# Kernel optimization log

Measured on AMD Instinct MI355X. Metric: run time of the kernel, lower is better.

The kernel has to match this reference:

```python
import jax, jax.numpy as jnp
import numpy as np

N_NODES = 100000
N_EDGES = 1200000
D_IN = 64
D_HID = 64


def setup_inputs() -> dict:
    key = jax.random.key(0)
    k1, k2, k3, k4, k5 = jax.random.split(key, 5)
    src = jax.random.randint(k1, (N_EDGES,), 0, N_NODES, dtype=jnp.int32)
    dst = jax.random.randint(k2, (N_EDGES,), 0, N_NODES, dtype=jnp.int32)
    w = jax.random.uniform(k3, (N_EDGES,), dtype=jnp.float32)
    data = jax.random.normal(k4, (N_NODES, D_IN), dtype=jnp.float32)
    theta = jax.random.normal(k5, (D_IN, D_HID), dtype=jnp.float32)
    return {"src": src, "dst": dst, "w": w, "data": data, "theta": theta,
            "num_nodes": N_NODES}


def reference(src, dst, w, data, theta, num_nodes):
    # weighted gather of source-node features: [E, D_IN]
    weighted = w[:, None] * data[src]
    # scatter-add into destination nodes: [N, D_IN]
    agg = jax.ops.segment_sum(weighted, dst, num_segments=num_nodes)
    # dense projection: [N, D_HID]
    return jnp.dot(agg, theta)
```

## Files before the change

kernel.cpp:

```cpp
#include <hip/hip_runtime.h>

#define D 64
#define NPB 128
#define NPB_SHIFT 7
#define MAXB 1024
#define SCATTER_T 512
#define CHUNK_MAX 4704
#define SCQ 10
#define CAPB 2560
#define GT 512
#define GQ 5

__device__ inline unsigned f2bf(float f) {
    unsigned u = __float_as_uint(f);
    return (u + 0x7FFFu + ((u >> 16) & 1u)) >> 16;
}

__global__ void zero_i_kernel(int* __restrict__ p, int n) {
    int i = blockIdx.x * blockDim.x + threadIdx.x;
    if (i < n) p[i] = 0;
}
__global__ void zero_f4_kernel(float4* __restrict__ p, int n4) {
    int i = blockIdx.x * blockDim.x + threadIdx.x;
    if (i < n4) p[i] = make_float4(0.f, 0.f, 0.f, 0.f);
}

__global__ __launch_bounds__(SCATTER_T) void bucket_scatter_kernel(
        const int* __restrict__ src, const int* __restrict__ dst,
        const float* __restrict__ w, int* __restrict__ cursor,
        int* __restrict__ ovfCnt, int4* __restrict__ ovf,
        int2* __restrict__ adjB, int E, int B) {
    __shared__ int lc[MAXB];
    __shared__ int lpre[MAXB];
    __shared__ int lbase[MAXB];
    __shared__ int lfill[MAXB];
    __shared__ int sums[SCATTER_T];
    __shared__ unsigned short sb[CHUNK_MAX];
    __shared__ int2 stage[CHUNK_MAX];

    int t = threadIdx.x;
    int chunk = (E + gridDim.x - 1) / gridDim.x;
    int lo = blockIdx.x * chunk, hi = min(lo + chunk, E);
    int n = hi - lo;
    if (n <= 0) return;

    for (int i = t; i < MAXB; i += SCATTER_T) { lc[i] = 0; lfill[i] = 0; }

    int rd[SCQ]; int rs[SCQ]; float rw[SCQ];
#pragma unroll
    for (int q = 0; q < SCQ; ++q) {
        int e = lo + t + q * SCATTER_T;
        bool v = e < hi;
        rd[q] = v ? dst[e] : -1;
        rs[q] = v ? src[e] : 0;
        rw[q] = v ? w[e] : 0.f;
    }
    __syncthreads();

#pragma unroll
    for (int q = 0; q < SCQ; ++q)
        if (rd[q] >= 0) atomicAdd(&lc[rd[q] >> NPB_SHIFT], 1);
    __syncthreads();

    int s0 = lc[2 * t], s1 = lc[2 * t + 1];
    sums[t] = s0 + s1;
    __syncthreads();
    for (int st = 1; st < SCATTER_T; st <<= 1) {
        int v = (t >= st) ? sums[t - st] : 0;
        __syncthreads();
        sums[t] += v;
        __syncthreads();
    }
    int ex = (t == 0) ? 0 : sums[t - 1];
    lpre[2 * t] = ex;
    lpre[2 * t + 1] = ex + s0;
    __syncthreads();

    for (int i = t; i < B; i += SCATTER_T) {
        int c = lc[i];
        lbase[i] = c ? atomicAdd(&cursor[i], c) : 0;
    }
    __syncthreads();

#pragma unroll
    for (int q = 0; q < SCQ; ++q) {
        int d = rd[q];
        if (d >= 0) {
            int bkt = d >> NPB_SHIFT;
            int i = lpre[bkt] + atomicAdd(&lfill[bkt], 1);
            stage[i] = make_int2(rs[q] | ((d & (NPB - 1)) << 20),
                                 __float_as_int(rw[q]));
            sb[i] = (unsigned short)bkt;
        }
    }
    __syncthreads();

    for (int i = t; i < n; i += SCATTER_T) {
        int bkt = sb[i];
        int2 v = stage[i];
        int pos = lbase[bkt] + (i - lpre[bkt]);
        if (pos < CAPB) {
            adjB[(size_t)bkt * CAPB + pos] = v;
        } else {
            int oi = atomicAdd(ovfCnt, 1);
            ovf[oi] = make_int4(v.x, v.y, bkt, 0);
        }
    }
}

__global__ __launch_bounds__(GT) void sort_gather_kernel(
        const int2* __restrict__ adjB, const int* __restrict__ cursor,
        const int* __restrict__ ovfCnt, const int4* __restrict__ ovf,
        const unsigned* __restrict__ projU, float* __restrict__ out, int N) {
    __shared__ int cnt[NPB];
    __shared__ int pre[NPB];
    __shared__ int fill[NPB];
    __shared__ int2 ladj[CAPB];
    __shared__ int sOvf;

    int b = blockIdx.x;
    int t = threadIdx.x;
    int total = cursor[b];
    int m = min(total, CAPB);
    const int2* base = adjB + (size_t)b * CAPB;

    if (t < NPB) { cnt[t] = 0; fill[t] = 0; }
    if (t == 0) sOvf = *ovfCnt;
    __syncthreads();

    int2 r[GQ];
#pragma unroll
    for (int q = 0; q < GQ; ++q) {
        int e = t + q * GT;
        if (e < m) {
            int2 a = base[e];
            r[q] = a;
            atomicAdd(&cnt[((unsigned)a.x) >> 20], 1);
        }
    }
    __syncthreads();
    if (t < NPB) pre[t] = cnt[t];
    __syncthreads();
    for (int st = 1; st < NPB; st <<= 1) {
        int v = (t < NPB && t >= st) ? pre[t - st] : 0;
        __syncthreads();
        if (t < NPB) pre[t] += v;
        __syncthreads();
    }
#pragma unroll
    for (int q = 0; q < GQ; ++q) {
        int e = t + q * GT;
        if (e < m) {
            int2 a = r[q];
            int dL = ((unsigned)a.x) >> 20;
            int pos = ((dL == 0) ? 0 : pre[dL - 1]) + atomicAdd(&fill[dL], 1);
            ladj[pos] = make_int2(a.x & 0xFFFFF, a.y);
        }
    }
    __syncthreads();

    int wave = t >> 6;
    int lane = t & 63;
    int half = lane >> 5;
    int k = lane & 31;

#pragma unroll 1
    for (int i = 0; i < 8; ++i) {
        int dL = wave * 16 + i * 2 + half;
        int node = b * NPB + dL;
        if (node < N) {
            int rb = (dL == 0) ? 0 : pre[dL - 1];
            int re = pre[dL];
            float2 accA = make_float2(0.f, 0.f);
            float2 accB = make_float2(0.f, 0.f);
            int j = rb;
            for (; j + 3 < re; j += 4) {
                int2 a0 = ladj[j];
                int2 a1 = ladj[j + 1];
                int2 a2 = ladj[j + 2];
                int2 a3 = ladj[j + 3];
                unsigned p0 = projU[(size_t)a0.x * 32 + k];
                unsigned p1 = projU[(size_t)a1.x * 32 + k];
                unsigned p2 = projU[(size_t)a2.x * 32 + k];
                unsigned p3 = projU[(size_t)a3.x * 32 + k];
                float w0 = __int_as_float(a0.y), w1 = __int_as_float(a1.y);
                float w2 = __int_as_float(a2.y), w3 = __int_as_float(a3.y);
                accA.x += w0 * __uint_as_float(p0 << 16);
                accA.y += w0 * __uint_as_float(p0 & 0xFFFF0000u);
                accB.x += w1 * __uint_as_float(p1 << 16);
                accB.y += w1 * __uint_as_float(p1 & 0xFFFF0000u);
                accA.x += w2 * __uint_as_float(p2 << 16);
                accA.y += w2 * __uint_as_float(p2 & 0xFFFF0000u);
                accB.x += w3 * __uint_as_float(p3 << 16);
                accB.y += w3 * __uint_as_float(p3 & 0xFFFF0000u);
            }
            for (; j < re; ++j) {
                int2 a0 = ladj[j];
                float w0 = __int_as_float(a0.y);
                unsigned p0 = projU[(size_t)a0.x * 32 + k];
                accA.x += w0 * __uint_as_float(p0 << 16);
                accA.y += w0 * __uint_as_float(p0 & 0xFFFF0000u);
            }
            float2 acc = make_float2(accA.x + accB.x, accA.y + accB.y);
            *(float2*)&out[(size_t)node * D + 2 * k] = acc;
        }
    }

    if (sOvf > 0) {
        __syncthreads();
        for (int e = t; e < sOvf; e += GT) {
            int4 o = ovf[e];
            if (o.z != b) continue;
            int dL = ((unsigned)o.x) >> 20;
            int node = b * NPB + dL;
            if (node >= N) continue;
            float wgt = __int_as_float(o.y);
            int s = o.x & 0xFFFFF;
            for (int d2 = 0; d2 < D / 2; ++d2) {
                unsigned p = projU[(size_t)s * 32 + d2];
                atomicAdd(&out[(size_t)node * D + 2 * d2],     wgt * __uint_as_float(p << 16));
                atomicAdd(&out[(size_t)node * D + 2 * d2 + 1], wgt * __uint_as_float(p & 0xFFFF0000u));
            }
        }
    }
}

__global__ __launch_bounds__(256, 4) void rowgemm_bf16_kernel(const float* __restrict__ A,
                                                              const float* __restrict__ theta,
                                                              unsigned short* __restrict__ proj16,
                                                              int N) {
    __shared__ float th[D * D];
    __shared__ float at[D][68];
    int t = threadIdx.x;
    int rowBase = blockIdx.x * 64;

#pragma unroll
    for (int i = 0; i < 4; ++i) {
        int f = t + i * 256;
        ((float4*)th)[f] = ((const float4*)theta)[f];
    }
#pragma unroll
    for (int i = 0; i < 4; ++i) {
        int f = t + i * 256;
        int row = f >> 4;
        int kv = f & 15;
        float4 v = make_float4(0.f, 0.f, 0.f, 0.f);
        if (rowBase + row < N) v = *(const float4*)&A[(size_t)(rowBase + row) * D + kv * 4];
        at[kv * 4 + 0][row] = v.x;
        at[kv * 4 + 1][row] = v.y;
        at[kv * 4 + 2][row] = v.z;
        at[kv * 4 + 3][row] = v.w;
    }
    __syncthreads();

    int c0 = (t & 15) * 4;
    int r0 = (t >> 4) * 4;
    float4 acc0 = make_float4(0.f, 0.f, 0.f, 0.f);
    float4 acc1 = acc0, acc2 = acc0, acc3 = acc0;

#pragma unroll 16
    for (int k = 0; k < D; ++k) {
        float4 bv = *(const float4*)&th[k * D + c0];
        float4 av = *(const float4*)&at[k][r0];
        acc0.x += av.x * bv.x; acc0.y += av.x * bv.y; acc0.z += av.x * bv.z; acc0.w += av.x * bv.w;
        acc1.x += av.y * bv.x; acc1.y += av.y * bv.y; acc1.z += av.y * bv.z; acc1.w += av.y * bv.w;
        acc2.x += av.z * bv.x; acc2.y += av.z * bv.y; acc2.z += av.z * bv.z; acc2.w += av.z * bv.w;
        acc3.x += av.w * bv.x; acc3.y += av.w * bv.y; acc3.z += av.w * bv.z; acc3.w += av.w * bv.w;
    }

    float4 accs[4] = {acc0, acc1, acc2, acc3};
#pragma unroll
    for (int i = 0; i < 4; ++i) {
        int r = rowBase + r0 + i;
        if (r < N) {
            unsigned lo = f2bf(accs[i].x) | (f2bf(accs[i].y) << 16);
            unsigned hi = f2bf(accs[i].z) | (f2bf(accs[i].w) << 16);
            *(uint2*)&proj16[(size_t)r * D + c0] = make_uint2(lo, hi);
        }
    }
}

__global__ void scatter_kernel(const int* __restrict__ src, const int* __restrict__ dst,
                               const float* __restrict__ w, const float* __restrict__ data,
                               float* __restrict__ agg, int E) {
    int tid = blockIdx.x * blockDim.x + threadIdx.x;
    int e = tid >> 6;
    int d = tid & 63;
    if (e >= E) return;
    float val = w[e] * data[(size_t)src[e] * D + d];
    atomicAdd(&agg[(size_t)dst[e] * D + d], val);
}

__global__ __launch_bounds__(256, 4) void rowgemm_f32_kernel(const float* __restrict__ A,
                                                             const float* __restrict__ theta,
                                                             float* __restrict__ out, int N) {
    __shared__ float th[D * D];
    __shared__ float at[D][68];
    int t = threadIdx.x;
    int rowBase = blockIdx.x * 64;
#pragma unroll
    for (int i = 0; i < 4; ++i) {
        int f = t + i * 256;
        ((float4*)th)[f] = ((const float4*)theta)[f];
    }
#pragma unroll
    for (int i = 0; i < 4; ++i) {
        int f = t + i * 256;
        int row = f >> 4;
        int kv = f & 15;
        float4 v = make_float4(0.f, 0.f, 0.f, 0.f);
        if (rowBase + row < N) v = *(const float4*)&A[(size_t)(rowBase + row) * D + kv * 4];
        at[kv * 4 + 0][row] = v.x;
        at[kv * 4 + 1][row] = v.y;
        at[kv * 4 + 2][row] = v.z;
        at[kv * 4 + 3][row] = v.w;
    }
    __syncthreads();
    int c0 = (t & 15) * 4;
    int r0 = (t >> 4) * 4;
    float4 acc0 = make_float4(0.f, 0.f, 0.f, 0.f);
    float4 acc1 = acc0, acc2 = acc0, acc3 = acc0;
#pragma unroll 16
    for (int kk = 0; kk < D; ++kk) {
        float4 bv = *(const float4*)&th[kk * D + c0];
        float4 av = *(const float4*)&at[kk][r0];
        acc0.x += av.x * bv.x; acc0.y += av.x * bv.y; acc0.z += av.x * bv.z; acc0.w += av.x * bv.w;
        acc1.x += av.y * bv.x; acc1.y += av.y * bv.y; acc1.z += av.y * bv.z; acc1.w += av.y * bv.w;
        acc2.x += av.z * bv.x; acc2.y += av.z * bv.y; acc2.z += av.z * bv.z; acc2.w += av.z * bv.w;
        acc3.x += av.w * bv.x; acc3.y += av.w * bv.y; acc3.z += av.w * bv.z; acc3.w += av.w * bv.w;
    }
    float4 accs[4] = {acc0, acc1, acc2, acc3};
#pragma unroll
    for (int i = 0; i < 4; ++i) {
        int r = rowBase + r0 + i;
        if (r < N) *(float4*)&out[(size_t)r * D + c0] = accs[i];
    }
}

extern "C" void kernel_launch(void* const* d_in, const int* in_sizes, int n_in,
                              void* d_out, int out_size, void* d_ws, size_t ws_size,
                              hipStream_t stream) {
    const int*   src   = (const int*)d_in[0];
    const int*   dst   = (const int*)d_in[1];
    const float* w     = (const float*)d_in[2];
    const float* data  = (const float*)d_in[3];
    const float* theta = (const float*)d_in[4];
    const int E = in_sizes[0];
    const int N = in_sizes[3] / D;
    float* out = (float*)d_out;

    const int B = (N + NPB - 1) / NPB;

    size_t projBytes = (size_t)N * D * 2;
    size_t adjBytes  = (size_t)B * CAPB * 8;
    size_t ovfBytes  = (size_t)E * 16;
    size_t need = projBytes + adjBytes + ovfBytes + ((size_t)B + 1) * 4 + 256;

    if (ws_size >= need && N < (1 << 20) && B <= MAXB) {
        unsigned short* proj16 = (unsigned short*)d_ws;
        int2* adjB   = (int2*)((char*)d_ws + projBytes);
        int4* ovf    = (int4*)((char*)d_ws + projBytes + adjBytes);
        int*  cursor = (int*)((char*)d_ws + projBytes + adjBytes + ovfBytes);
        int*  ovfCnt = cursor + B;

        int gs = (E + CHUNK_MAX - 1) / CHUNK_MAX;

        zero_i_kernel<<<(B + 1 + 255) / 256, 256, 0, stream>>>(cursor, B + 1);
        bucket_scatter_kernel<<<gs, SCATTER_T, 0, stream>>>(src, dst, w, cursor,
                                                            ovfCnt, ovf, adjB, E, B);
        rowgemm_bf16_kernel<<<(N + 63) / 64, 256, 0, stream>>>(data, theta, proj16, N);
        sort_gather_kernel<<<B, GT, 0, stream>>>(adjB, cursor, ovfCnt, ovf,
                                                 (const unsigned*)proj16, out, N);
    } else {
        float* agg = (float*)d_ws;
        int n4 = (N * D) / 4;
        zero_f4_kernel<<<(n4 + 255) / 256, 256, 0, stream>>>((float4*)agg, n4);
        long long total = (long long)E * D;
        scatter_kernel<<<(int)((total + 255) / 256), 256, 0, stream>>>(src, dst, w, data, agg, E);
        rowgemm_f32_kernel<<<(N + 63) / 64, 256, 0, stream>>>(agg, theta, out, N);
    }
}
```

Measured before the change: 146.1 us.

## Fold cursor zeroing into GEMM, wave-shuffle scan, smaller scatter chunks, unroll gather

```diff
diff --git a/kernel.cpp b/kernel.cpp
--- a/kernel.cpp
+++ b/kernel.cpp
@@ -5,8 +5,8 @@
 #define NPB_SHIFT 7
 #define MAXB 1024
 #define SCATTER_T 512
-#define CHUNK_MAX 4704
-#define SCQ 10
+#define CHUNK_MAX 2352
+#define SCQ 5
 #define CAPB 2560
 #define GT 512
 #define GQ 5
@@ -16,10 +16,6 @@
     return (u + 0x7FFFu + ((u >> 16) & 1u)) >> 16;
 }
 
-__global__ void zero_i_kernel(int* __restrict__ p, int n) {
-    int i = blockIdx.x * blockDim.x + threadIdx.x;
-    if (i < n) p[i] = 0;
-}
 __global__ void zero_f4_kernel(float4* __restrict__ p, int n4) {
     int i = blockIdx.x * blockDim.x + threadIdx.x;
     if (i < n4) p[i] = make_float4(0.f, 0.f, 0.f, 0.f);
@@ -34,7 +30,8 @@
     __shared__ int lpre[MAXB];
     __shared__ int lbase[MAXB];
     __shared__ int lfill[MAXB];
-    __shared__ int sums[SCATTER_T];
+    __shared__ int wsum[8];
+    __shared__ int wexc[8];
     __shared__ unsigned short sb[CHUNK_MAX];
     __shared__ int2 stage[CHUNK_MAX];
 
@@ -63,17 +60,25 @@
     __syncthreads();
 
     int s0 = lc[2 * t], s1 = lc[2 * t + 1];
-    sums[t] = s0 + s1;
-    __syncthreads();
-    for (int st = 1; st < SCATTER_T; st <<= 1) {
-        int v = (t >= st) ? sums[t - st] : 0;
-        __syncthreads();
-        sums[t] += v;
-        __syncthreads();
-    }
-    int ex = (t == 0) ? 0 : sums[t - 1];
-    lpre[2 * t] = ex;
-    lpre[2 * t + 1] = ex + s0;
+    int tsum = s0 + s1;
+    int lane = t & 63, wid = t >> 6;
+    int v = tsum;
+#pragma unroll
+    for (int off = 1; off < 64; off <<= 1) {
+        int u = __shfl_up(v, off, 64);
+        if (lane >= off) v += u;
+    }
+    if (lane == 63) wsum[wid] = v;
+    __syncthreads();
+    if (t < 8) {
+        int acc = 0;
+        for (int i = 0; i < t; ++i) acc += wsum[i];
+        wexc[t] = acc;
+    }
+    __syncthreads();
+    int base = wexc[wid] + (v - tsum);
+    lpre[2 * t] = base;
+    lpre[2 * t + 1] = base + s0;
     __syncthreads();
 
     for (int i = t; i < B; i += SCATTER_T) {
@@ -97,13 +102,13 @@
 
     for (int i = t; i < n; i += SCATTER_T) {
         int bkt = sb[i];
-        int2 v = stage[i];
+        int2 vv = stage[i];
         int pos = lbase[bkt] + (i - lpre[bkt]);
         if (pos < CAPB) {
-            adjB[(size_t)bkt * CAPB + pos] = v;
+            adjB[(size_t)bkt * CAPB + pos] = vv;
         } else {
             int oi = atomicAdd(ovfCnt, 1);
-            ovf[oi] = make_int4(v.x, v.y, bkt, 0);
+            ovf[oi] = make_int4(vv.x, vv.y, bkt, 0);
         }
     }
 }
@@ -174,6 +179,44 @@
             float2 accA = make_float2(0.f, 0.f);
             float2 accB = make_float2(0.f, 0.f);
             int j = rb;
+            for (; j + 7 < re; j += 8) {
+                int2 a0 = ladj[j];
+                int2 a1 = ladj[j + 1];
+                int2 a2 = ladj[j + 2];
+                int2 a3 = ladj[j + 3];
+                int2 a4 = ladj[j + 4];
+                int2 a5 = ladj[j + 5];
+                int2 a6 = ladj[j + 6];
+                int2 a7 = ladj[j + 7];
+                unsigned p0 = projU[(size_t)a0.x * 32 + k];
+                unsigned p1 = projU[(size_t)a1.x * 32 + k];
+                unsigned p2 = projU[(size_t)a2.x * 32 + k];
+                unsigned p3 = projU[(size_t)a3.x * 32 + k];
+                unsigned p4 = projU[(size_t)a4.x * 32 + k];
+                unsigned p5 = projU[(size_t)a5.x * 32 + k];
+                unsigned p6 = projU[(size_t)a6.x * 32 + k];
+                unsigned p7 = projU[(size_t)a7.x * 32 + k];
+                float w0 = __int_as_float(a0.y), w1 = __int_as_float(a1.y);
+                float w2 = __int_as_float(a2.y), w3 = __int_as_float(a3.y);
+                float w4 = __int_as_float(a4.y), w5 = __int_as_float(a5.y);
+                float w6 = __int_as_float(a6.y), w7 = __int_as_float(a7.y);
+                accA.x += w0 * __uint_as_float(p0 << 16);
+                accA.y += w0 * __uint_as_float(p0 & 0xFFFF0000u);
+                accB.x += w1 * __uint_as_float(p1 << 16);
+                accB.y += w1 * __uint_as_float(p1 & 0xFFFF0000u);
+                accA.x += w2 * __uint_as_float(p2 << 16);
+                accA.y += w2 * __uint_as_float(p2 & 0xFFFF0000u);
+                accB.x += w3 * __uint_as_float(p3 << 16);
+                accB.y += w3 * __uint_as_float(p3 & 0xFFFF0000u);
+                accA.x += w4 * __uint_as_float(p4 << 16);
+                accA.y += w4 * __uint_as_float(p4 & 0xFFFF0000u);
+                accB.x += w5 * __uint_as_float(p5 << 16);
+                accB.y += w5 * __uint_as_float(p5 & 0xFFFF0000u);
+                accA.x += w6 * __uint_as_float(p6 << 16);
+                accA.y += w6 * __uint_as_float(p6 & 0xFFFF0000u);
+                accB.x += w7 * __uint_as_float(p7 << 16);
+                accB.y += w7 * __uint_as_float(p7 & 0xFFFF0000u);
+            }
             for (; j + 3 < re; j += 4) {
                 int2 a0 = ladj[j];
                 int2 a1 = ladj[j + 1];
@@ -228,11 +271,15 @@
 __global__ __launch_bounds__(256, 4) void rowgemm_bf16_kernel(const float* __restrict__ A,
                                                               const float* __restrict__ theta,
                                                               unsigned short* __restrict__ proj16,
-                                                              int N) {
+                                                              int* __restrict__ cursor,
+                                                              int nCur, int N) {
     __shared__ float th[D * D];
     __shared__ float at[D][68];
     int t = threadIdx.x;
     int rowBase = blockIdx.x * 64;
+
+    if (blockIdx.x == 0)
+        for (int i = t; i < nCur; i += 256) cursor[i] = 0;
 
 #pragma unroll
     for (int i = 0; i < 4; ++i) {
@@ -365,10 +412,10 @@
 
         int gs = (E + CHUNK_MAX - 1) / CHUNK_MAX;
 
-        zero_i_kernel<<<(B + 1 + 255) / 256, 256, 0, stream>>>(cursor, B + 1);
+        rowgemm_bf16_kernel<<<(N + 63) / 64, 256, 0, stream>>>(data, theta, proj16,
+                                                               cursor, B + 1, N);
         bucket_scatter_kernel<<<gs, SCATTER_T, 0, stream>>>(src, dst, w, cursor,
                                                             ovfCnt, ovf, adjB, E, B);
-        rowgemm_bf16_kernel<<<(N + 63) / 64, 256, 0, stream>>>(data, theta, proj16, N);
         sort_gather_kernel<<<B, GT, 0, stream>>>(adjB, cursor, ovfCnt, ovf,
                                                  (const unsigned*)proj16, out, N);
     } else {
```

After: 150.1 us. +2.7%, slower.
